# Kernel tuning notes

Measured on AMD Instinct MI355X. Metric: run time of the kernel, lower is better.

The kernel has to match this reference:

```python
import jax, jax.numpy as jnp
import numpy as np
import math

B, S, E, H = 2, 2048, 1024, 16
D = E // H  # head_dim = 64


def setup_inputs() -> dict:
    key = jax.random.key(0)
    ks = jax.random.split(key, 12)
    scale = 1.0 / math.sqrt(E)
    inp = {
        "q": jax.random.normal(ks[0], (B, S, E), jnp.float32),
        "k": jax.random.normal(ks[1], (B, S, E), jnp.float32),
        "v": jax.random.normal(ks[2], (B, S, E), jnp.float32),
        # causal mask, broadcast over batch and heads
        "mask": jnp.tril(jnp.ones((S, S), jnp.bool_))[None, None, :, :],
        "Wq": jax.random.normal(ks[3], (E, E), jnp.float32) * scale,
        "bq": jnp.zeros((E,), jnp.float32),
        "Wk": jax.random.normal(ks[4], (E, E), jnp.float32) * scale,
        "bk": jnp.zeros((E,), jnp.float32),
        "Wv": jax.random.normal(ks[5], (E, E), jnp.float32) * scale,
        "bv": jnp.zeros((E,), jnp.float32),
        "Wo": jax.random.normal(ks[6], (E, E), jnp.float32) * scale,
        "bo": jnp.zeros((E,), jnp.float32),
    }
    return inp


def _heads(x, W, b):
    # nn.Linear: x @ W.T + b, then split into heads -> [B, H, S, D]
    y = x @ W.T + b
    return y.reshape(B, S, H, D).transpose(0, 2, 1, 3)


def reference(q, k, v, mask, Wq, bq, Wk, bk, Wv, bv, Wo, bo):
    qh = _heads(q, Wq, bq)   # [B,H,S,D]
    kh = _heads(k, Wk, bk)
    vh = _heads(v, Wv, bv)
    scores = jnp.einsum("bhqd,bhkd->bhqk", qh, kh) / math.sqrt(D)
    scores = jnp.where(mask, scores, -1e9)
    probs = jax.nn.softmax(scores, axis=-1)  # dropout is identity in eval
    ctx = jnp.einsum("bhqk,bhkd->bhqd", probs, vh)
    ctx = ctx.transpose(0, 2, 1, 3).reshape(B, S, E)
    return ctx @ Wo.T + bo
```

## Files before the change

### kernel.cpp

```cpp
#include <hip/hip_runtime.h>
#include <hip/hip_bf16.h>
#include <cstdint>

#define PB 2
#define PS 2048
#define PE 1024
#define PH 16
#define PD 64

typedef __attribute__((ext_vector_type(8))) short short8;
typedef __attribute__((ext_vector_type(8))) ushort u16x8;
typedef __attribute__((ext_vector_type(4))) float f32x4;

static __device__ __forceinline__ float bf2f(ushort u) {
  return __uint_as_float(((unsigned)u) << 16);
}
static __device__ __forceinline__ ushort f2bf(float f) {
  unsigned u = __float_as_uint(f);
  u += 0x7fffu + ((u >> 16) & 1u);
  return (ushort)(u >> 16);
}
static __device__ __forceinline__ unsigned pkbf(float a, float b) {
  __hip_bfloat162 h = __float22bfloat162_rn(make_float2(a, b));
  return *reinterpret_cast<unsigned*>(&h);
}
static __device__ __forceinline__ u16x8 cvt8(f32x4 a, f32x4 b) {
  union { unsigned u[4]; u16x8 v; } r;
  r.u[0] = pkbf(a[0], a[1]); r.u[1] = pkbf(a[2], a[3]);
  r.u[2] = pkbf(b[0], b[1]); r.u[3] = pkbf(b[2], b[3]);
  return r.v;
}

static __device__ __forceinline__ void async16(void* lds, const void* g) {
  __attribute__((address_space(3))) unsigned* l =
      reinterpret_cast<__attribute__((address_space(3))) unsigned*>(
          reinterpret_cast<uintptr_t>(lds));
  const __attribute__((address_space(1))) unsigned* gp =
      reinterpret_cast<const __attribute__((address_space(1))) unsigned*>(
          reinterpret_cast<uintptr_t>(g));
  __builtin_amdgcn_global_load_lds(gp, l, 16, 0, 0);
}

__global__ __launch_bounds__(256)
void cvt_kernel(const float* __restrict__ s0, const float* __restrict__ s1,
                const float* __restrict__ s2, const float* __restrict__ s3,
                const float* __restrict__ s4, const float* __restrict__ s5,
                const float* __restrict__ s6,
                ushort* d0, ushort* d1, ushort* d2, ushort* d3, ushort* d4,
                ushort* d5, ushort* d6) {
  const int t = blockIdx.y;
  const float* src = t == 0 ? s0 : t == 1 ? s1 : t == 2 ? s2 : t == 3 ? s3
                   : t == 4 ? s4 : t == 5 ? s5 : s6;
  ushort* dst = t == 0 ? d0 : t == 1 ? d1 : t == 2 ? d2 : t == 3 ? d3
              : t == 4 ? d4 : t == 5 ? d5 : d6;
  const size_t n = (t < 3) ? (size_t)4194304 : (size_t)1048576;
  const size_t i0 = ((size_t)blockIdx.x * 256 + threadIdx.x) * 8;
  if (i0 >= n) return;
  const f32x4 a = *(const f32x4*)(src + i0);
  const f32x4 b = *(const f32x4*)(src + i0 + 4);
  *(u16x8*)(dst + i0) = cvt8(a, b);
}

template <bool SWAP>
__device__ __forceinline__ void gemm_core(const ushort* __restrict__ A,
                                          const ushort* __restrict__ W,
                                          int m0, int n0,
                                          ushort* As, ushort* Bs,
                                          f32x4 acc[4][4]) {
  const int tid  = threadIdx.x;
  const int wave = tid >> 6;
  const int lane = tid & 63;
  const int quad = lane >> 4;
  const int lrow = lane & 15;
  const int wm = wave >> 1;
  const int wn = wave & 1;
  const int row0 = tid >> 2;
  const int kc8  = (tid & 3) * 8;

  for (int kt = 0; kt < PE; kt += 32) {
    async16(As + (size_t)wave * 512,        A + (size_t)(m0 + row0)      * PE + kt + kc8);
    async16(As + 2048 + (size_t)wave * 512, A + (size_t)(m0 + row0 + 64) * PE + kt + kc8);
    async16(Bs + (size_t)wave * 512,        W + (size_t)(n0 + row0)      * PE + kt + kc8);
    async16(Bs + 2048 + (size_t)wave * 512, W + (size_t)(n0 + row0 + 64) * PE + kt + kc8);
    __syncthreads();
    short8 af[4], bf[4];
#pragma unroll
    for (int i = 0; i < 4; ++i) {
      af[i] = *(const short8*)(As + (wm * 64 + i * 16 + lrow) * 32 + quad * 8);
      bf[i] = *(const short8*)(Bs + (wn * 64 + i * 16 + lrow) * 32 + quad * 8);
    }
#pragma unroll
    for (int i = 0; i < 4; ++i)
#pragma unroll
      for (int j = 0; j < 4; ++j) {
        if (SWAP)
          acc[i][j] = __builtin_amdgcn_mfma_f32_16x16x32_bf16(bf[j], af[i], acc[i][j], 0, 0, 0);
        else
          acc[i][j] = __builtin_amdgcn_mfma_f32_16x16x32_bf16(af[i], bf[j], acc[i][j], 0, 0, 0);
      }
    __syncthreads();
  }
}

__global__ __launch_bounds__(256)
void qkv_kernel(const ushort* __restrict__ q, const ushort* __restrict__ k,
                const ushort* __restrict__ v,
                const ushort* __restrict__ Wq, const ushort* __restrict__ Wk,
                const ushort* __restrict__ Wv,
                const float* __restrict__ bq, const float* __restrict__ bk,
                const float* __restrict__ bv,
                ushort* __restrict__ qh, ushort* __restrict__ kh,
                ushort* __restrict__ vt) {
  __shared__ __align__(16) ushort As[128 * 32];
  __shared__ __align__(16) ushort Bs[128 * 32];
  const int which = blockIdx.y >> 3;
  const int n0 = (blockIdx.y & 7) * 128;
  const int m0 = blockIdx.x * 128;
  const ushort* A  = which == 0 ? q  : (which == 1 ? k  : v);
  const ushort* W  = which == 0 ? Wq : (which == 1 ? Wk : Wv);
  const float* bi  = which == 0 ? bq : (which == 1 ? bk : bv);

  const int lane = threadIdx.x & 63;
  const int wave = threadIdx.x >> 6;
  const int quad = lane >> 4, lrow = lane & 15;
  const int wm = wave >> 1, wn = wave & 1;

  f32x4 acc[4][4] = {};
  if (which == 2) {
    gemm_core<true>(A, W, m0, n0, As, Bs, acc);
#pragma unroll
    for (int j = 0; j < 4; ++j) {
#pragma unroll
      for (int i = 0; i < 4; ++i) {
        const int xrow = m0 + wm * 64 + i * 16 + lrow;
        const int b = xrow >> 11, s = xrow & 2047;
#pragma unroll
        for (int r = 0; r < 4; ++r) {
          const int dcol = n0 + wn * 64 + j * 16 + quad * 4 + r;
          const int h = dcol >> 6, d = dcol & 63;
          vt[((size_t)((b << 4) + h) << 17) + ((size_t)d << 11) + s] =
              f2bf(acc[i][j][r] + bi[dcol]);
        }
      }
    }
  } else {
    gemm_core<false>(A, W, m0, n0, As, Bs, acc);
    ushort* Out = which == 0 ? qh : kh;
#pragma unroll
    for (int j = 0; j < 4; ++j) {
      const int col = n0 + wn * 64 + j * 16 + lrow;
      const float bias = bi[col];
      const int h = col >> 6, d = col & 63;
#pragma unroll
      for (int i = 0; i < 4; ++i)
#pragma unroll
        for (int r = 0; r < 4; ++r) {
          const int row = m0 + wm * 64 + i * 16 + quad * 4 + r;
          const int b = row >> 11, s = row & 2047;
          Out[((size_t)((b << 4) + h) << 17) + ((size_t)s << 6) + d] =
              f2bf(acc[i][j][r] + bias);
        }
    }
  }
}

__global__ __launch_bounds__(256)
void outproj_kernel(const ushort* __restrict__ ctx, const ushort* __restrict__ Wo,
                    const float* __restrict__ bo, float* __restrict__ out) {
  __shared__ __align__(16) ushort As[128 * 32];
  __shared__ __align__(16) ushort Bs[128 * 32];
  const int n0 = blockIdx.y * 128;
  const int m0 = blockIdx.x * 128;

  f32x4 acc[4][4] = {};
  gemm_core<false>(ctx, Wo, m0, n0, As, Bs, acc);

  const int lane = threadIdx.x & 63;
  const int wave = threadIdx.x >> 6;
  const int quad = lane >> 4, lrow = lane & 15;
  const int wm = wave >> 1, wn = wave & 1;
#pragma unroll
  for (int j = 0; j < 4; ++j) {
    const int col = n0 + wn * 64 + j * 16 + lrow;
    const float bias = bo[col];
#pragma unroll
    for (int i = 0; i < 4; ++i)
#pragma unroll
      for (int r = 0; r < 4; ++r) {
        const int row = m0 + wm * 64 + i * 16 + quad * 4 + r;
        out[((size_t)row << 10) + col] = acc[i][j][r] + bias;
      }
  }
}

#define SW_IDX(r, g) (((r) << 6) + ((((g) ^ ((r) & 7))) << 3))
#define QSCALE 0.180336879f

__global__ __launch_bounds__(256)
void attn_kernel(const ushort* __restrict__ qh, const ushort* __restrict__ kh,
                 const ushort* __restrict__ vt, ushort* __restrict__ ctx) {
  __shared__ __align__(16) ushort Ks[2][4096];
  __shared__ __align__(16) ushort Vs[2][4096];
  __shared__ __align__(16) ushort Ps[4][1024];
  const int tid  = threadIdx.x;
  const int wave = tid >> 6;
  const int lane = tid & 63;
  const int quad = lane >> 4;
  const int lrow = lane & 15;
  const int bh = blockIdx.x, b = bh >> 4, h = bh & 15;
  const size_t base = (size_t)bh << 17;
  const int srow = tid >> 2;
  const int sg0  = (tid & 3) * 2;
  const int pr   = wave * 16 + lrow;
  ushort* Pw = &Ps[wave][0];
  const int prow = lrow << 6;

  const int qb = 31 - blockIdx.y;
  const int q0 = qb * 64;

  short8 qf0, qf1;
  {
    const ushort* qp = qh + base + (size_t)(q0 + pr) * 64 + quad * 8;
    const u16x8 a = *(const u16x8*)qp;
    const u16x8 c = *(const u16x8*)(qp + 32);
#pragma unroll
    for (int j = 0; j < 8; ++j) {
      qf0[j] = (short)f2bf(bf2f(a[j]) * QSCALE);
      qf1[j] = (short)f2bf(bf2f(c[j]) * QSCALE);
    }
  }

  f32x4 o_acc[4] = {};
  float m_i = -1e30f, l_i = 0.f;

  u16x8 kst0, kst1, vst0, vst1;
  {
    const ushort* kp = kh + base + (size_t)srow * 64 + sg0 * 8;
    kst0 = *(const u16x8*)kp; kst1 = *(const u16x8*)(kp + 8);
    const ushort* vp = vt + base + (size_t)srow * 2048 + sg0 * 8;
    vst0 = *(const u16x8*)vp; vst1 = *(const u16x8*)(vp + 8);
  }

  for (int kt = 0; kt <= qb; ++kt) {
    const int buf = kt & 1;
    *(u16x8*)&Ks[buf][SW_IDX(srow, sg0)]     = kst0;
    *(u16x8*)&Ks[buf][SW_IDX(srow, sg0 + 1)] = kst1;
    *(u16x8*)&Vs[buf][SW_IDX(srow, sg0)]     = vst0;
    *(u16x8*)&Vs[buf][SW_IDX(srow, sg0 + 1)] = vst1;
    __syncthreads();

    if (kt < qb) {
      const ushort* kp = kh + base + (size_t)((kt + 1) * 64 + srow) * 64 + sg0 * 8;
      kst0 = *(const u16x8*)kp; kst1 = *(const u16x8*)(kp + 8);
      const ushort* vp = vt + base + (size_t)srow * 2048 + (kt + 1) * 64 + sg0 * 8;
      vst0 = *(const u16x8*)vp; vst1 = *(const u16x8*)(vp + 8);
    }

    f32x4 st[4] = {};
#pragma unroll
    for (int nt = 0; nt < 4; ++nt) {
      const int r = nt * 16 + lrow;
      const short8 kb0 = *(const short8*)&Ks[buf][SW_IDX(r, quad)];
      const short8 kb1 = *(const short8*)&Ks[buf][SW_IDX(r, quad + 4)];
      st[nt] = __builtin_amdgcn_mfma_f32_16x16x32_bf16(kb0, qf0, st[nt], 0, 0, 0);
      st[nt] = __builtin_amdgcn_mfma_f32_16x16x32_bf16(kb1, qf1, st[nt], 0, 0, 0);
    }

    if (kt == qb) {
#pragma unroll
      for (int nt = 0; nt < 4; ++nt)
#pragma unroll
        for (int r = 0; r < 4; ++r)
          if (nt * 16 + quad * 4 + r > pr) st[nt][r] = -1e30f;
    }

    float rm = -1e30f;
#pragma unroll
    for (int nt = 0; nt < 4; ++nt)
#pragma unroll
      for (int r = 0; r < 4; ++r) rm = fmaxf(rm, st[nt][r]);
    rm = fmaxf(rm, __shfl_xor(rm, 16));
    rm = fmaxf(rm, __shfl_xor(rm, 32));
    const float mn = fmaxf(m_i, rm);
    const float alpha = exp2f(m_i - mn);
    m_i = mn;
    float rs = 0.f;
#pragma unroll
    for (int nt = 0; nt < 4; ++nt) {
      float p0 = exp2f(st[nt][0] - mn);
      float p1 = exp2f(st[nt][1] - mn);
      float p2 = exp2f(st[nt][2] - mn);
      float p3 = exp2f(st[nt][3] - mn);
      rs += (p0 + p1) + (p2 + p3);
      uint2 pk;
      pk.x = pkbf(p0, p1); pk.y = pkbf(p2, p3);
      *(uint2*)&Pw[prow + (((nt * 2 + (quad >> 1)) ^ (lrow & 7)) << 3) +
                   (quad & 1) * 4] = pk;
    }
    rs += __shfl_xor(rs, 16);
    rs += __shfl_xor(rs, 32);
    l_i = l_i * alpha + rs;
#pragma unroll
    for (int nt = 0; nt < 4; ++nt) o_acc[nt] *= alpha;

    const short8 pa0 = *(const short8*)&Pw[prow + ((quad ^ (lrow & 7)) << 3)];
    const short8 pa1 = *(const short8*)&Pw[prow + (((quad + 4) ^ (lrow & 7)) << 3)];
#pragma unroll
    for (int nt = 0; nt < 4; ++nt) {
      const int r = nt * 16 + lrow;
      const short8 vb0 = *(const short8*)&Vs[buf][SW_IDX(r, quad)];
      const short8 vb1 = *(const short8*)&Vs[buf][SW_IDX(r, quad + 4)];
      o_acc[nt] = __builtin_amdgcn_mfma_f32_16x16x32_bf16(vb0, pa0, o_acc[nt], 0, 0, 0);
      o_acc[nt] = __builtin_amdgcn_mfma_f32_16x16x32_bf16(vb1, pa1, o_acc[nt], 0, 0, 0);
    }
  }

  const float inv = 1.f / l_i;
  const size_t rowb = ((size_t)b << 21) + ((size_t)(q0 + pr) << 10) + (h << 6);
#pragma unroll
  for (int nt = 0; nt < 4; ++nt) {
    uint2 u;
    u.x = pkbf(o_acc[nt][0] * inv, o_acc[nt][1] * inv);
    u.y = pkbf(o_acc[nt][2] * inv, o_acc[nt][3] * inv);
    *(uint2*)(ctx + rowb + nt * 16 + quad * 4) = u;
  }
}

extern "C" void kernel_launch(void* const* d_in, const int* in_sizes, int n_in,
                              void* d_out, int out_size, void* d_ws, size_t ws_size,
                              hipStream_t stream) {
  const float* q  = (const float*)d_in[0];
  const float* k  = (const float*)d_in[1];
  const float* v  = (const float*)d_in[2];
  const float* Wq = (const float*)d_in[4];
  const float* bq = (const float*)d_in[5];
  const float* Wk = (const float*)d_in[6];
  const float* bk = (const float*)d_in[7];
  const float* Wv = (const float*)d_in[8];
  const float* bv = (const float*)d_in[9];
  const float* Wo = (const float*)d_in[10];
  const float* bo = (const float*)d_in[11];

  const size_t NTOK = (size_t)PB * PS * PE;
  const size_t NW   = (size_t)PE * PE;
  ushort* qh  = (ushort*)d_ws;
  ushort* kh  = qh + NTOK;
  ushort* vt  = kh + NTOK;
  ushort* qc  = vt + NTOK;
  ushort* kc  = qc + NTOK;
  ushort* vc  = kc + NTOK;
  ushort* wqc = vc + NTOK;
  ushort* wkc = wqc + NW;
  ushort* wvc = wkc + NW;
  ushort* woc = wvc + NW;
  ushort* ctx = qc;

  cvt_kernel<<<dim3(2048, 7), dim3(256), 0, stream>>>(
      q, k, v, Wq, Wk, Wv, Wo, qc, kc, vc, wqc, wkc, wvc, woc);
  qkv_kernel<<<dim3(32, 24), dim3(256), 0, stream>>>(
      qc, kc, vc, wqc, wkc, wvc, bq, bk, bv, qh, kh, vt);
  attn_kernel<<<dim3(32, 32), dim3(256), 0, stream>>>(qh, kh, vt, ctx);
  outproj_kernel<<<dim3(32, 8), dim3(256), 0, stream>>>(
      ctx, woc, bo, (float*)d_out);
}
```

Before: 240.6 us.

## Process two query tiles per attention block and widen conversion per thread

```diff
diff --git a/kernel.cpp b/kernel.cpp
--- a/kernel.cpp
+++ b/kernel.cpp
@@ -54,11 +54,14 @@
   ushort* dst = t == 0 ? d0 : t == 1 ? d1 : t == 2 ? d2 : t == 3 ? d3
               : t == 4 ? d4 : t == 5 ? d5 : d6;
   const size_t n = (t < 3) ? (size_t)4194304 : (size_t)1048576;
-  const size_t i0 = ((size_t)blockIdx.x * 256 + threadIdx.x) * 8;
+  const size_t i0 = ((size_t)blockIdx.x * 256 + threadIdx.x) * 16;
   if (i0 >= n) return;
   const f32x4 a = *(const f32x4*)(src + i0);
   const f32x4 b = *(const f32x4*)(src + i0 + 4);
+  const f32x4 c = *(const f32x4*)(src + i0 + 8);
+  const f32x4 d = *(const f32x4*)(src + i0 + 12);
   *(u16x8*)(dst + i0) = cvt8(a, b);
+  *(u16x8*)(dst + i0 + 8) = cvt8(c, d);
 }
 
 template <bool SWAP>
@@ -201,7 +204,7 @@
                  const ushort* __restrict__ vt, ushort* __restrict__ ctx) {
   __shared__ __align__(16) ushort Ks[2][4096];
   __shared__ __align__(16) ushort Vs[2][4096];
-  __shared__ __align__(16) ushort Ps[4][1024];
+  __shared__ __align__(16) ushort Ps[4][2048];
   const int tid  = threadIdx.x;
   const int wave = tid >> 6;
   const int lane = tid & 63;
@@ -212,26 +215,34 @@
   const int srow = tid >> 2;
   const int sg0  = (tid & 3) * 2;
   const int pr   = wave * 16 + lrow;
-  ushort* Pw = &Ps[wave][0];
+  ushort* PwA = &Ps[wave][0];
+  ushort* PwB = &Ps[wave][1024];
   const int prow = lrow << 6;
 
-  const int qb = 31 - blockIdx.y;
-  const int q0 = qb * 64;
-
-  short8 qf0, qf1;
+  const int p = 15 - blockIdx.y;
+  const int q0 = p * 128;
+  const int diagA = 2 * p;
+  const int ktmax = 2 * p + 1;
+
+  short8 qfA0, qfA1, qfB0, qfB1;
   {
-    const ushort* qp = qh + base + (size_t)(q0 + pr) * 64 + quad * 8;
-    const u16x8 a = *(const u16x8*)qp;
-    const u16x8 c = *(const u16x8*)(qp + 32);
+    const ushort* qa = qh + base + (size_t)(q0 + pr) * 64 + quad * 8;
+    const ushort* qb2 = qa + (size_t)64 * 64;
+    const u16x8 a0 = *(const u16x8*)qa;
+    const u16x8 a1 = *(const u16x8*)(qa + 32);
+    const u16x8 b0 = *(const u16x8*)qb2;
+    const u16x8 b1 = *(const u16x8*)(qb2 + 32);
 #pragma unroll
     for (int j = 0; j < 8; ++j) {
-      qf0[j] = (short)f2bf(bf2f(a[j]) * QSCALE);
-      qf1[j] = (short)f2bf(bf2f(c[j]) * QSCALE);
-    }
-  }
-
-  f32x4 o_acc[4] = {};
-  float m_i = -1e30f, l_i = 0.f;
+      qfA0[j] = (short)f2bf(bf2f(a0[j]) * QSCALE);
+      qfA1[j] = (short)f2bf(bf2f(a1[j]) * QSCALE);
+      qfB0[j] = (short)f2bf(bf2f(b0[j]) * QSCALE);
+      qfB1[j] = (short)f2bf(bf2f(b1[j]) * QSCALE);
+    }
+  }
+
+  f32x4 oA[4] = {}, oB[4] = {};
+  float mA = -1e30f, lA = 0.f, mB = -1e30f, lB = 0.f;
 
   u16x8 kst0, kst1, vst0, vst1;
   {
@@ -241,7 +252,7 @@
     vst0 = *(const u16x8*)vp; vst1 = *(const u16x8*)(vp + 8);
   }
 
-  for (int kt = 0; kt <= qb; ++kt) {
+  for (int kt = 0; kt <= ktmax; ++kt) {
     const int buf = kt & 1;
     *(u16x8*)&Ks[buf][SW_IDX(srow, sg0)]     = kst0;
     *(u16x8*)&Ks[buf][SW_IDX(srow, sg0 + 1)] = kst1;
@@ -249,80 +260,147 @@
     *(u16x8*)&Vs[buf][SW_IDX(srow, sg0 + 1)] = vst1;
     __syncthreads();
 
-    if (kt < qb) {
+    if (kt < ktmax) {
       const ushort* kp = kh + base + (size_t)((kt + 1) * 64 + srow) * 64 + sg0 * 8;
       kst0 = *(const u16x8*)kp; kst1 = *(const u16x8*)(kp + 8);
       const ushort* vp = vt + base + (size_t)srow * 2048 + (kt + 1) * 64 + sg0 * 8;
       vst0 = *(const u16x8*)vp; vst1 = *(const u16x8*)(vp + 8);
     }
 
-    f32x4 st[4] = {};
+    const bool doA = (kt <= diagA);
+
+    f32x4 stA[4] = {}, stB[4] = {};
 #pragma unroll
     for (int nt = 0; nt < 4; ++nt) {
       const int r = nt * 16 + lrow;
       const short8 kb0 = *(const short8*)&Ks[buf][SW_IDX(r, quad)];
       const short8 kb1 = *(const short8*)&Ks[buf][SW_IDX(r, quad + 4)];
-      st[nt] = __builtin_amdgcn_mfma_f32_16x16x32_bf16(kb0, qf0, st[nt], 0, 0, 0);
-      st[nt] = __builtin_amdgcn_mfma_f32_16x16x32_bf16(kb1, qf1, st[nt], 0, 0, 0);
-    }
-
-    if (kt == qb) {
+      stB[nt] = __builtin_amdgcn_mfma_f32_16x16x32_bf16(kb0, qfB0, stB[nt], 0, 0, 0);
+      stB[nt] = __builtin_amdgcn_mfma_f32_16x16x32_bf16(kb1, qfB1, stB[nt], 0, 0, 0);
+      if (doA) {
+        stA[nt] = __builtin_amdgcn_mfma_f32_16x16x32_bf16(kb0, qfA0, stA[nt], 0, 0, 0);
+        stA[nt] = __builtin_amdgcn_mfma_f32_16x16x32_bf16(kb1, qfA1, stA[nt], 0, 0, 0);
+      }
+    }
+
+    if (kt == diagA) {
 #pragma unroll
       for (int nt = 0; nt < 4; ++nt)
 #pragma unroll
         for (int r = 0; r < 4; ++r)
-          if (nt * 16 + quad * 4 + r > pr) st[nt][r] = -1e30f;
-    }
-
-    float rm = -1e30f;
-#pragma unroll
-    for (int nt = 0; nt < 4; ++nt)
-#pragma unroll
-      for (int r = 0; r < 4; ++r) rm = fmaxf(rm, st[nt][r]);
-    rm = fmaxf(rm, __shfl_xor(rm, 16));
-    rm = fmaxf(rm, __shfl_xor(rm, 32));
-    const float mn = fmaxf(m_i, rm);
-    const float alpha = exp2f(m_i - mn);
-    m_i = mn;
-    float rs = 0.f;
-#pragma unroll
-    for (int nt = 0; nt < 4; ++nt) {
-      float p0 = exp2f(st[nt][0] - mn);
-      float p1 = exp2f(st[nt][1] - mn);
-      float p2 = exp2f(st[nt][2] - mn);
-      float p3 = exp2f(st[nt][3] - mn);
-      rs += (p0 + p1) + (p2 + p3);
-      uint2 pk;
-      pk.x = pkbf(p0, p1); pk.y = pkbf(p2, p3);
-      *(uint2*)&Pw[prow + (((nt * 2 + (quad >> 1)) ^ (lrow & 7)) << 3) +
-                   (quad & 1) * 4] = pk;
-    }
-    rs += __shfl_xor(rs, 16);
-    rs += __shfl_xor(rs, 32);
-    l_i = l_i * alpha + rs;
-#pragma unroll
-    for (int nt = 0; nt < 4; ++nt) o_acc[nt] *= alpha;
-
-    const short8 pa0 = *(const short8*)&Pw[prow + ((quad ^ (lrow & 7)) << 3)];
-    const short8 pa1 = *(const short8*)&Pw[prow + (((quad + 4) ^ (lrow & 7)) << 3)];
+          if (nt * 16 + quad * 4 + r > pr) stA[nt][r] = -1e30f;
+    }
+    if (kt == diagA + 1) {
+#pragma unroll
+      for (int nt = 0; nt < 4; ++nt)
+#pragma unroll
+        for (int r = 0; r < 4; ++r)
+          if (nt * 16 + quad * 4 + r > pr) stB[nt][r] = -1e30f;
+    }
+
+    {
+      float rm = -1e30f;
+#pragma unroll
+      for (int nt = 0; nt < 4; ++nt)
+#pragma unroll
+        for (int r = 0; r < 4; ++r) rm = fmaxf(rm, stB[nt][r]);
+      rm = fmaxf(rm, __shfl_xor(rm, 16));
+      rm = fmaxf(rm, __shfl_xor(rm, 32));
+      const float mn = fmaxf(mB, rm);
+      const float alpha = exp2f(mB - mn);
+      mB = mn;
+      float rs = 0.f;
+#pragma unroll
+      for (int nt = 0; nt < 4; ++nt) {
+        float p0 = exp2f(stB[nt][0] - mn);
+        float p1 = exp2f(stB[nt][1] - mn);
+        float p2 = exp2f(stB[nt][2] - mn);
+        float p3 = exp2f(stB[nt][3] - mn);
+        rs += (p0 + p1) + (p2 + p3);
+        uint2 pk;
+        pk.x = pkbf(p0, p1); pk.y = pkbf(p2, p3);
+        *(uint2*)&PwB[prow + (((nt * 2 + (quad >> 1)) ^ (lrow & 7)) << 3) +
+                      (quad & 1) * 4] = pk;
+      }
+      rs += __shfl_xor(rs, 16);
+      rs += __shfl_xor(rs, 32);
+      lB = lB * alpha + rs;
+#pragma unroll
+      for (int nt = 0; nt < 4; ++nt) oB[nt] *= alpha;
+    }
+    if (doA) {
+      float rm = -1e30f;
+#pragma unroll
+      for (int nt = 0; nt < 4; ++nt)
+#pragma unroll
+        for (int r = 0; r < 4; ++r) rm = fmaxf(rm, stA[nt][r]);
+      rm = fmaxf(rm, __shfl_xor(rm, 16));
+      rm = fmaxf(rm, __shfl_xor(rm, 32));
+      const float mn = fmaxf(mA, rm);
+      const float alpha = exp2f(mA - mn);
+      mA = mn;
+      float rs = 0.f;
+#pragma unroll
+      for (int nt = 0; nt < 4; ++nt) {
+        float p0 = exp2f(stA[nt][0] - mn);
+        float p1 = exp2f(stA[nt][1] - mn);
+        float p2 = exp2f(stA[nt][2] - mn);
+        float p3 = exp2f(stA[nt][3] - mn);
+        rs += (p0 + p1) + (p2 + p3);
+        uint2 pk;
+        pk.x = pkbf(p0, p1); pk.y = pkbf(p2, p3);
+        *(uint2*)&PwA[prow + (((nt * 2 + (quad >> 1)) ^ (lrow & 7)) << 3) +
+                      (quad & 1) * 4] = pk;
+      }
+      rs += __shfl_xor(rs, 16);
+      rs += __shfl_xor(rs, 32);
+      lA = lA * alpha + rs;
+#pragma unroll
+      for (int nt = 0; nt < 4; ++nt) oA[nt] *= alpha;
+    }
+
+    const short8 paB0 = *(const short8*)&PwB[prow + ((quad ^ (lrow & 7)) << 3)];
+    const short8 paB1 = *(const short8*)&PwB[prow + (((quad + 4) ^ (lrow & 7)) << 3)];
+    short8 paA0, paA1;
+    if (doA) {
+      paA0 = *(const short8*)&PwA[prow + ((quad ^ (lrow & 7)) << 3)];
+      paA1 = *(const short8*)&PwA[prow + (((quad + 4) ^ (lrow & 7)) << 3)];
+    }
 #pragma unroll
     for (int nt = 0; nt < 4; ++nt) {
       const int r = nt * 16 + lrow;
       const short8 vb0 = *(const short8*)&Vs[buf][SW_IDX(r, quad)];
       const short8 vb1 = *(const short8*)&Vs[buf][SW_IDX(r, quad + 4)];
-      o_acc[nt] = __builtin_amdgcn_mfma_f32_16x16x32_bf16(vb0, pa0, o_acc[nt], 0, 0, 0);
-      o_acc[nt] = __builtin_amdgcn_mfma_f32_16x16x32_bf16(vb1, pa1, o_acc[nt], 0, 0, 0);
-    }
-  }
-
-  const float inv = 1.f / l_i;
-  const size_t rowb = ((size_t)b << 21) + ((size_t)(q0 + pr) << 10) + (h << 6);
-#pragma unroll
-  for (int nt = 0; nt < 4; ++nt) {
-    uint2 u;
-    u.x = pkbf(o_acc[nt][0] * inv, o_acc[nt][1] * inv);
-    u.y = pkbf(o_acc[nt][2] * inv, o_acc[nt][3] * inv);
-    *(uint2*)(ctx + rowb + nt * 16 + quad * 4) = u;
+      oB[nt] = __builtin_amdgcn_mfma_f32_16x16x32_bf16(vb0, paB0, oB[nt], 0, 0, 0);
+      oB[nt] = __builtin_amdgcn_mfma_f32_16x16x32_bf16(vb1, paB1, oB[nt], 0, 0, 0);
+      if (doA) {
+        oA[nt] = __builtin_amdgcn_mfma_f32_16x16x32_bf16(vb0, paA0, oA[nt], 0, 0, 0);
+        oA[nt] = __builtin_amdgcn_mfma_f32_16x16x32_bf16(vb1, paA1, oA[nt], 0, 0, 0);
+      }
+    }
+  }
+
+  {
+    const float inv = 1.f / lA;
+    const size_t rowb = ((size_t)b << 21) + ((size_t)(q0 + pr) << 10) + (h << 6);
+#pragma unroll
+    for (int nt = 0; nt < 4; ++nt) {
+      uint2 u;
+      u.x = pkbf(oA[nt][0] * inv, oA[nt][1] * inv);
+      u.y = pkbf(oA[nt][2] * inv, oA[nt][3] * inv);
+      *(uint2*)(ctx + rowb + nt * 16 + quad * 4) = u;
+    }
+  }
+  {
+    const float inv = 1.f / lB;
+    const size_t rowb = ((size_t)b << 21) + ((size_t)(q0 + 64 + pr) << 10) + (h << 6);
+#pragma unroll
+    for (int nt = 0; nt < 4; ++nt) {
+      uint2 u;
+      u.x = pkbf(oB[nt][0] * inv, oB[nt][1] * inv);
+      u.y = pkbf(oB[nt][2] * inv, oB[nt][3] * inv);
+      *(uint2*)(ctx + rowb + nt * 16 + quad * 4) = u;
+    }
   }
 }
 
@@ -355,11 +433,11 @@
   ushort* woc = wvc + NW;
   ushort* ctx = qc;
 
-  cvt_kernel<<<dim3(2048, 7), dim3(256), 0, stream>>>(
+  cvt_kernel<<<dim3(1024, 7), dim3(256), 0, stream>>>(
       q, k, v, Wq, Wk, Wv, Wo, qc, kc, vc, wqc, wkc, wvc, woc);
   qkv_kernel<<<dim3(32, 24), dim3(256), 0, stream>>>(
       qc, kc, vc, wqc, wkc, wvc, bq, bk, bv, qh, kh, vt);
-  attn_kernel<<<dim3(32, 32), dim3(256), 0, stream>>>(qh, kh, vt, ctx);
+  attn_kernel<<<dim3(32, 16), dim3(256), 0, stream>>>(qh, kh, vt, ctx);
   outproj_kernel<<<dim3(32, 8), dim3(256), 0, stream>>>(
       ctx, woc, bo, (float*)d_out);
 }
```

Result: slower. 270.5 us (+12.4%).
